# Kernel optimization log

Hardware: AMD Instinct MI355X
Metric: run time of the kernel (lower is better)

The kernel has to match this reference:

```python
import jax, jax.numpy as jnp
import numpy as np

B, J, T = 64, 24, 2048
FOOT_IDX = (7, 8, 10, 11)
LAMBDA_VEL = 0.2
LAMBDA_FOOT = 0.1
CONTACT_THRESH = 0.05


def setup_inputs() -> dict:
    key = jax.random.key(0)
    k1, k2, k3 = jax.random.split(key, 3)
    pred = jax.random.normal(k1, (B, J, 6, T), dtype=jnp.float32)
    target = jax.random.normal(k2, (B, J, 6, T), dtype=jnp.float32)
    joint_positions = jax.random.normal(k3, (B, J, 3, T), dtype=jnp.float32)
    return {"pred": pred, "target": target, "joint_positions": joint_positions}


def _foot_contact_loss(joint_positions):
    # joint_positions: [B, J, 3, T]
    foot_pos = joint_positions[:, jnp.array(FOOT_IDX), :, :]        # [B, F, 3, T]
    foot_height = foot_pos[:, :, 1, :]                              # [B, F, T]
    contact_w = jax.nn.sigmoid((CONTACT_THRESH - foot_height) * 20.0)
    foot_vel = foot_pos[:, :, :, 1:] - foot_pos[:, :, :, :-1]       # [B, F, 3, T-1]
    foot_vel_xz = foot_vel[:, :, jnp.array([0, 2]), :]              # [B, F, 2, T-1]
    cw_vel = (contact_w[:, :, 1:] + contact_w[:, :, :-1]) * 0.5     # [B, F, T-1]
    loss = (foot_vel_xz ** 2).sum(axis=2) * cw_vel                  # [B, F, T-1]
    num_contacts = cw_vel.sum() + 1e-8
    return loss.sum() / num_contacts


def reference(pred, target, joint_positions):
    # Reconstruction MSE on 6D rotations
    recon = jnp.mean((pred - target) ** 2)
    # First-order velocity loss over frames (last axis)
    dp = pred[:, :, :, 1:] - pred[:, :, :, :-1]
    dt = target[:, :, :, 1:] - target[:, :, :, :-1]
    vel = jnp.mean((dp - dt) ** 2)
    # Foot contact (anti-sliding) loss
    foot = _foot_contact_loss(joint_positions)
    total = recon + LAMBDA_VEL * vel + LAMBDA_FOOT * foot
    return total
```

## Files before the change

### kernel.cpp

```cpp
#include <hip/hip_runtime.h>

#define BB 64
#define JJ 24
#define TT 2048
#define NELEM (BB*JJ*6*TT)
#define NVEL  ((long long)BB*JJ*6*(TT-1))
#define FOOT_BLOCKS 256
#define RGRID 2048
#define NTH (RGRID*256)
#define NC4 (NELEM/4)
#define ITERS 9
#define NBLK (FOOT_BLOCKS + RGRID)

__device__ __forceinline__ void block_reduce2f(float& a, float& b) {
    #pragma unroll
    for (int off = 32; off > 0; off >>= 1) {
        a += __shfl_down(a, off);
        b += __shfl_down(b, off);
    }
    __shared__ float sa[4], sb[4];
    const int lane = threadIdx.x & 63;
    const int wid  = threadIdx.x >> 6;
    if (lane == 0) { sa[wid] = a; sb[wid] = b; }
    __syncthreads();
    if (threadIdx.x == 0) {
        for (int w = 1; w < 4; ++w) { a += sa[w]; b += sb[w]; }
    }
}

__device__ __forceinline__ float sigm(float y) {
    return 1.f / (1.f + __expf(-(0.05f - y) * 20.f));
}

__global__ __launch_bounds__(256) void fused_kernel(
        const float* __restrict__ pred, const float* __restrict__ targ,
        const float* __restrict__ jp, double2* __restrict__ parts) {

    if (blockIdx.x < FOOT_BLOCKS) {
        const int FI[4] = {7, 8, 10, 11};
        const int bf = blockIdx.x;
        const int b  = bf >> 2;
        const int j  = FI[bf & 3];
        const float* __restrict__ xrow = jp + ((size_t)(b * JJ + j) * 3) * TT;
        const float* __restrict__ yrow = xrow + TT;
        const float* __restrict__ zrow = xrow + 2 * TT;
        const float4* __restrict__ x4 = reinterpret_cast<const float4*>(xrow);
        const float4* __restrict__ y4 = reinterpret_cast<const float4*>(yrow);
        const float4* __restrict__ z4 = reinterpret_cast<const float4*>(zrow);

        float lsum = 0.f, csum = 0.f;
        #pragma unroll
        for (int cc = 0; cc < 2; ++cc) {
            const int c = threadIdx.x + cc * 256;
            const float4 xv = x4[c], yv = y4[c], zv = z4[c];
            float x0 = 0.f, y0 = 0.f, z0 = 0.f;
            if (c > 0) { x0 = xrow[4*c-1]; y0 = yrow[4*c-1]; z0 = zrow[4*c-1]; }
            const float w0 = sigm(y0),  w1 = sigm(yv.x), w2 = sigm(yv.y),
                        w3 = sigm(yv.z), w4 = sigm(yv.w);
            auto term = [&](float x1, float xp, float z1, float zp,
                            float wa, float wb) {
                const float cw = 0.5f * (wa + wb);
                const float vx = x1 - xp, vz = z1 - zp;
                lsum += (vx * vx + vz * vz) * cw;
                csum += cw;
            };
            if (c > 0) term(xv.x, x0, zv.x, z0, w1, w0);
            term(xv.y, xv.x, zv.y, zv.x, w2, w1);
            term(xv.z, xv.y, zv.z, zv.y, w3, w2);
            term(xv.w, xv.z, zv.w, zv.z, w4, w3);
        }
        block_reduce2f(lsum, csum);
        if (threadIdx.x == 0)
            parts[blockIdx.x] = make_double2((double)lsum, (double)csum);
    } else {
        const int t = (blockIdx.x - FOOT_BLOCKS) * 256 + threadIdx.x;
        const float4* __restrict__ pred4 = reinterpret_cast<const float4*>(pred);
        const float4* __restrict__ targ4 = reinterpret_cast<const float4*>(targ);
        const bool hasb  = (t & 511) != 0;
        const bool lead  = (threadIdx.x & 63) == 0;

        float4 P0 = pred4[t], G0 = targ4[t];
        float pmg0 = 0.f;
        if (lead && hasb) pmg0 = pred[4*t - 1] - targ[4*t - 1];

        float recon = 0.f, vel = 0.f;
        #pragma unroll 1
        for (int k = 0; k < ITERS; ++k) {
            float4 P1, G1;
            float pmg1 = 0.f;
            if (k + 1 < ITERS) {
                const int c = t + (k + 1) * NTH;
                P1 = pred4[c];
                G1 = targ4[c];
                if (lead && hasb) pmg1 = pred[4*c - 1] - targ[4*c - 1];
            }

            const float d0 = P0.x - G0.x, d1 = P0.y - G0.y,
                        d2 = P0.z - G0.z, d3 = P0.w - G0.w;
            recon += d0*d0 + d1*d1 + d2*d2 + d3*d3;
            const float e01 = d1 - d0, e12 = d2 - d1, e23 = d3 - d2;
            vel += e01*e01 + e12*e12 + e23*e23;

            float prev = __shfl_up(d3, 1);
            if (lead) prev = pmg0;
            if (hasb) { const float b0 = d0 - prev; vel += b0 * b0; }

            P0 = P1; G0 = G1; pmg0 = pmg1;
        }

        block_reduce2f(recon, vel);
        if (threadIdx.x == 0)
            parts[blockIdx.x] = make_double2((double)recon, (double)vel);
    }
}

__global__ __launch_bounds__(256) void finalize_kernel(
        const double2* __restrict__ parts, float* __restrict__ out) {
    double fl = 0.0, fc = 0.0, rc = 0.0, vl = 0.0;
    for (int i = threadIdx.x; i < NBLK; i += 256) {
        const double2 v = parts[i];
        if (i < FOOT_BLOCKS) { fl += v.x; fc += v.y; }
        else                 { rc += v.x; vl += v.y; }
    }
    #pragma unroll
    for (int off = 32; off > 0; off >>= 1) {
        rc += __shfl_down(rc, off);
        vl += __shfl_down(vl, off);
        fl += __shfl_down(fl, off);
        fc += __shfl_down(fc, off);
    }
    __shared__ double s4[4][4];
    const int lane = threadIdx.x & 63, wid = threadIdx.x >> 6;
    if (lane == 0) { s4[wid][0]=rc; s4[wid][1]=vl; s4[wid][2]=fl; s4[wid][3]=fc; }
    __syncthreads();
    if (threadIdx.x == 0) {
        for (int w = 1; w < 4; ++w) {
            rc += s4[w][0]; vl += s4[w][1]; fl += s4[w][2]; fc += s4[w][3];
        }
        const double r = rc / (double)NELEM;
        const double v = vl / (double)NVEL;
        const double f = fl / (fc + 1e-8);
        out[0] = (float)(r + 0.2 * v + 0.1 * f);
    }
}

extern "C" void kernel_launch(void* const* d_in, const int* in_sizes, int n_in,
                              void* d_out, int out_size, void* d_ws, size_t ws_size,
                              hipStream_t stream) {
    const float* pred = (const float*)d_in[0];
    const float* targ = (const float*)d_in[1];
    const float* jp   = (const float*)d_in[2];
    float* out     = (float*)d_out;
    double2* parts = (double2*)d_ws;

    fused_kernel<<<NBLK, 256, 0, stream>>>(pred, targ, jp, parts);
    finalize_kernel<<<1, 256, 0, stream>>>(parts, out);
}
```

Before: 189.3 us.

## Spread foot-contact work across all reduction blocks and drop separate foot blocks

Removes the 256 dedicated foot-contact blocks. Every main reduction block now also handles one 256-frame segment of one foot row, using scalar loads with one timestep per thread. The manual software-prefetch double buffering in the recon/velocity loop is replaced by a plain loop with unroll 3, which leaves load scheduling to the compiler. Partial sums become double4 per block, and a single 4-way block reduction replaces the two 2-way paths. This balances load and removes divergent block roles. The cost is unvectorized scalar jp loads and possibly less latency hiding in the main loop.

```diff
diff --git a/kernel.cpp b/kernel.cpp
--- a/kernel.cpp
+++ b/kernel.cpp
@@ -5,122 +5,100 @@
 #define TT 2048
 #define NELEM (BB*JJ*6*TT)
 #define NVEL  ((long long)BB*JJ*6*(TT-1))
-#define FOOT_BLOCKS 256
 #define RGRID 2048
 #define NTH (RGRID*256)
-#define NC4 (NELEM/4)
 #define ITERS 9
-#define NBLK (FOOT_BLOCKS + RGRID)
-
-__device__ __forceinline__ void block_reduce2f(float& a, float& b) {
-    #pragma unroll
-    for (int off = 32; off > 0; off >>= 1) {
-        a += __shfl_down(a, off);
-        b += __shfl_down(b, off);
-    }
-    __shared__ float sa[4], sb[4];
-    const int lane = threadIdx.x & 63;
-    const int wid  = threadIdx.x >> 6;
-    if (lane == 0) { sa[wid] = a; sb[wid] = b; }
-    __syncthreads();
-    if (threadIdx.x == 0) {
-        for (int w = 1; w < 4; ++w) { a += sa[w]; b += sb[w]; }
-    }
-}
+#define SEGT 256
 
 __device__ __forceinline__ float sigm(float y) {
     return 1.f / (1.f + __expf(-(0.05f - y) * 20.f));
 }
 
+__device__ __forceinline__ void block_reduce4f(float& a, float& b,
+                                               float& c, float& d) {
+    #pragma unroll
+    for (int off = 32; off > 0; off >>= 1) {
+        a += __shfl_down(a, off);
+        b += __shfl_down(b, off);
+        c += __shfl_down(c, off);
+        d += __shfl_down(d, off);
+    }
+    __shared__ float s[4][4];
+    const int lane = threadIdx.x & 63;
+    const int wid  = threadIdx.x >> 6;
+    if (lane == 0) { s[wid][0]=a; s[wid][1]=b; s[wid][2]=c; s[wid][3]=d; }
+    __syncthreads();
+    if (threadIdx.x == 0) {
+        for (int w = 1; w < 4; ++w) {
+            a += s[w][0]; b += s[w][1]; c += s[w][2]; d += s[w][3];
+        }
+    }
+}
+
 __global__ __launch_bounds__(256) void fused_kernel(
         const float* __restrict__ pred, const float* __restrict__ targ,
-        const float* __restrict__ jp, double2* __restrict__ parts) {
+        const float* __restrict__ jp, double4* __restrict__ parts) {
 
-    if (blockIdx.x < FOOT_BLOCKS) {
+    const int t = blockIdx.x * 256 + threadIdx.x;
+    const float4* __restrict__ pred4 = reinterpret_cast<const float4*>(pred);
+    const float4* __restrict__ targ4 = reinterpret_cast<const float4*>(targ);
+    const bool hasb = (t & 511) != 0;
+    const bool lead = (threadIdx.x & 63) == 0;
+
+    float footl = 0.f, footc = 0.f;
+    {
         const int FI[4] = {7, 8, 10, 11};
-        const int bf = blockIdx.x;
-        const int b  = bf >> 2;
-        const int j  = FI[bf & 3];
+        const int pair = blockIdx.x >> 3;
+        const int seg  = blockIdx.x & 7;
+        const int b    = pair >> 2;
+        const int j    = FI[pair & 3];
         const float* __restrict__ xrow = jp + ((size_t)(b * JJ + j) * 3) * TT;
         const float* __restrict__ yrow = xrow + TT;
         const float* __restrict__ zrow = xrow + 2 * TT;
-        const float4* __restrict__ x4 = reinterpret_cast<const float4*>(xrow);
-        const float4* __restrict__ y4 = reinterpret_cast<const float4*>(yrow);
-        const float4* __restrict__ z4 = reinterpret_cast<const float4*>(zrow);
+        const int tt = seg * SEGT + threadIdx.x;
+        if (tt >= 1) {
+            const float x1 = xrow[tt], x0 = xrow[tt - 1];
+            const float y1 = yrow[tt], y0 = yrow[tt - 1];
+            const float z1 = zrow[tt], z0 = zrow[tt - 1];
+            const float cw = 0.5f * (sigm(y1) + sigm(y0));
+            const float vx = x1 - x0, vz = z1 - z0;
+            footl = (vx * vx + vz * vz) * cw;
+            footc = cw;
+        }
+    }
 
-        float lsum = 0.f, csum = 0.f;
-        #pragma unroll
-        for (int cc = 0; cc < 2; ++cc) {
-            const int c = threadIdx.x + cc * 256;
-            const float4 xv = x4[c], yv = y4[c], zv = z4[c];
-            float x0 = 0.f, y0 = 0.f, z0 = 0.f;
-            if (c > 0) { x0 = xrow[4*c-1]; y0 = yrow[4*c-1]; z0 = zrow[4*c-1]; }
-            const float w0 = sigm(y0),  w1 = sigm(yv.x), w2 = sigm(yv.y),
-                        w3 = sigm(yv.z), w4 = sigm(yv.w);
-            auto term = [&](float x1, float xp, float z1, float zp,
-                            float wa, float wb) {
-                const float cw = 0.5f * (wa + wb);
-                const float vx = x1 - xp, vz = z1 - zp;
-                lsum += (vx * vx + vz * vz) * cw;
-                csum += cw;
-            };
-            if (c > 0) term(xv.x, x0, zv.x, z0, w1, w0);
-            term(xv.y, xv.x, zv.y, zv.x, w2, w1);
-            term(xv.z, xv.y, zv.z, zv.y, w3, w2);
-            term(xv.w, xv.z, zv.w, zv.z, w4, w3);
-        }
-        block_reduce2f(lsum, csum);
-        if (threadIdx.x == 0)
-            parts[blockIdx.x] = make_double2((double)lsum, (double)csum);
-    } else {
-        const int t = (blockIdx.x - FOOT_BLOCKS) * 256 + threadIdx.x;
-        const float4* __restrict__ pred4 = reinterpret_cast<const float4*>(pred);
-        const float4* __restrict__ targ4 = reinterpret_cast<const float4*>(targ);
-        const bool hasb  = (t & 511) != 0;
-        const bool lead  = (threadIdx.x & 63) == 0;
+    float recon = 0.f, vel = 0.f;
+    #pragma unroll 3
+    for (int k = 0; k < ITERS; ++k) {
+        const int c = t + k * NTH;
+        const float4 P = pred4[c];
+        const float4 G = targ4[c];
+        float pmg = 0.f;
+        if (lead && hasb) pmg = pred[4*c - 1] - targ[4*c - 1];
 
-        float4 P0 = pred4[t], G0 = targ4[t];
-        float pmg0 = 0.f;
-        if (lead && hasb) pmg0 = pred[4*t - 1] - targ[4*t - 1];
+        const float d0 = P.x - G.x, d1 = P.y - G.y,
+                    d2 = P.z - G.z, d3 = P.w - G.w;
+        recon += d0*d0 + d1*d1 + d2*d2 + d3*d3;
+        const float e01 = d1 - d0, e12 = d2 - d1, e23 = d3 - d2;
+        vel += e01*e01 + e12*e12 + e23*e23;
 
-        float recon = 0.f, vel = 0.f;
-        #pragma unroll 1
-        for (int k = 0; k < ITERS; ++k) {
-            float4 P1, G1;
-            float pmg1 = 0.f;
-            if (k + 1 < ITERS) {
-                const int c = t + (k + 1) * NTH;
-                P1 = pred4[c];
-                G1 = targ4[c];
-                if (lead && hasb) pmg1 = pred[4*c - 1] - targ[4*c - 1];
-            }
+        float prev = __shfl_up(d3, 1);
+        if (lead) prev = pmg;
+        if (hasb) { const float b0 = d0 - prev; vel += b0 * b0; }
+    }
 
-            const float d0 = P0.x - G0.x, d1 = P0.y - G0.y,
-                        d2 = P0.z - G0.z, d3 = P0.w - G0.w;
-            recon += d0*d0 + d1*d1 + d2*d2 + d3*d3;
-            const float e01 = d1 - d0, e12 = d2 - d1, e23 = d3 - d2;
-            vel += e01*e01 + e12*e12 + e23*e23;
-
-            float prev = __shfl_up(d3, 1);
-            if (lead) prev = pmg0;
-            if (hasb) { const float b0 = d0 - prev; vel += b0 * b0; }
-
-            P0 = P1; G0 = G1; pmg0 = pmg1;
-        }
-
-        block_reduce2f(recon, vel);
-        if (threadIdx.x == 0)
-            parts[blockIdx.x] = make_double2((double)recon, (double)vel);
-    }
+    block_reduce4f(recon, vel, footl, footc);
+    if (threadIdx.x == 0)
+        parts[blockIdx.x] = make_double4((double)recon, (double)vel,
+                                         (double)footl, (double)footc);
 }
 
 __global__ __launch_bounds__(256) void finalize_kernel(
-        const double2* __restrict__ parts, float* __restrict__ out) {
-    double fl = 0.0, fc = 0.0, rc = 0.0, vl = 0.0;
-    for (int i = threadIdx.x; i < NBLK; i += 256) {
-        const double2 v = parts[i];
-        if (i < FOOT_BLOCKS) { fl += v.x; fc += v.y; }
-        else                 { rc += v.x; vl += v.y; }
+        const double4* __restrict__ parts, float* __restrict__ out) {
+    double rc = 0.0, vl = 0.0, fl = 0.0, fc = 0.0;
+    for (int i = threadIdx.x; i < RGRID; i += 256) {
+        const double4 v = parts[i];
+        rc += v.x; vl += v.y; fl += v.z; fc += v.w;
     }
     #pragma unroll
     for (int off = 32; off > 0; off >>= 1) {
@@ -151,8 +129,8 @@
     const float* targ = (const float*)d_in[1];
     const float* jp   = (const float*)d_in[2];
     float* out     = (float*)d_out;
-    double2* parts = (double2*)d_ws;
+    double4* parts = (double4*)d_ws;
 
-    fused_kernel<<<NBLK, 256, 0, stream>>>(pred, targ, jp, parts);
+    fused_kernel<<<RGRID, 256, 0, stream>>>(pred, targ, jp, parts);
     finalize_kernel<<<1, 256, 0, stream>>>(parts, out);
 }
```

Result: no change. 187.6 us (-0.9%).
